# Kernel optimization log

Measured on AMD Instinct MI355X. Metric: run time of the kernel, lower is better.

## Reference

```python
import jax, jax.numpy as jnp
import numpy as np

B, L, ATTN, HID = 1024, 512, 1000, 1000

def setup_inputs() -> dict:
    key = jax.random.key(0)
    k = jax.random.split(key, 5)
    return {
        "hc": jax.random.normal(k[0], (B, HID), dtype=jnp.float32),
        "ho": jax.random.normal(k[1], (B, L, ATTN), dtype=jnp.float32),
        "mask": jnp.zeros((B, L), dtype=bool),
        "Wa_w": jax.random.normal(k[2], (1, ATTN), dtype=jnp.float32) / np.sqrt(ATTN),
        "Wa_b": jnp.zeros((1,), dtype=jnp.float32),
        "Wc_w": jax.random.normal(k[3], (HID, HID + ATTN), dtype=jnp.float32) / np.sqrt(HID + ATTN),
        "Wc_b": jnp.zeros((HID,), dtype=jnp.float32),
    }

def reference(hc, ho, mask, Wa_w, Wa_b, Wc_w, Wc_b):
    # scores: Wa(ho) -> [B, L], then mask + softmax over L
    scores = jnp.einsum('bld,od->bl', ho, Wa_w) + Wa_b[0]
    scores = jnp.where(mask, -10000.0, scores)
    a = jax.nn.softmax(scores, axis=-1)            # [B, L]
    c = jnp.einsum('bl,bld->bd', a, ho)            # context [B, ATTN]
    # dropout in eval mode (identity); concat + output projection
    h = jnp.concatenate([hc, c], axis=1) @ Wc_w.T + Wc_b  # [B, HID]
    return h
```

## Files before the change

### kernel.cpp

```cpp
#include <hip/hip_runtime.h>

#define NB 1024
#define NL 512
#define ND 1000
#define NH 1000

__device__ __forceinline__ void async_copy16(const void* g, void* l) {
    __builtin_amdgcn_global_load_lds(
        (const __attribute__((address_space(1))) void*)g,
        (__attribute__((address_space(3))) void*)l, 16, 0, 0);
}

__global__ __launch_bounds__(256, 4) void attn_pool_kernel(
    const float* __restrict__ ho,
    const unsigned char* __restrict__ mask,
    const float* __restrict__ Wa_w,
    const float* __restrict__ Wa_b,
    float* __restrict__ ctx)
{
    __shared__ __align__(16) char lbuf[4][2][4096];
    __shared__ unsigned char msk[NL];
    __shared__ float mArr[4], sArr[4];

    const int b    = blockIdx.x;
    const int tid  = threadIdx.x;
    const int wave = tid >> 6;
    const int lane = tid & 63;

    const unsigned char* mb = mask + (size_t)b * NL;
    msk[tid]       = mb[tid];
    msk[tid + 256] = mb[tid + 256];

    float4 wa[4];
    #pragma unroll
    for (int j = 0; j < 4; ++j) {
        int slot = lane + 64 * j;
        wa[j] = (slot < 250) ? ((const float4*)Wa_w)[slot] : make_float4(0.f, 0.f, 0.f, 0.f);
    }
    const float bias = Wa_b[0];

    const char* gb   = (const char*)(ho + (size_t)b * (NL * ND));
    const char* gend = (const char*)ho + ((size_t)NB * NL * ND) * 4 - 16;

    __syncthreads();

    auto stageRow = [&](int d, int l) {
        const char* rp = gb + (size_t)l * 4000;
        char* lb = &lbuf[wave][d][0];
        #pragma unroll
        for (int s4 = 0; s4 < 4; ++s4) {
            const char* p = rp + s4 * 1024 + lane * 16;
            if (p > gend) p = gend;
            async_copy16((const void*)p, (void*)(lb + s4 * 1024));
        }
    };

    float  m = -1e30f, s = 0.f;
    float4 acc[4];
    #pragma unroll
    for (int j = 0; j < 4; ++j) acc[j] = make_float4(0.f, 0.f, 0.f, 0.f);

    stageRow(0, wave);

    #pragma unroll 1
    for (int c = 0; c < 128; ++c) {
        if (c + 1 < 128) {
            stageRow((c + 1) & 1, 4 * (c + 1) + wave);
            asm volatile("s_waitcnt vmcnt(4)" ::: "memory");
        } else {
            asm volatile("s_waitcnt vmcnt(0)" ::: "memory");
        }
        __builtin_amdgcn_sched_barrier(0);

        const float4* row = (const float4*)&lbuf[wave][c & 1][0];
        float4 v[4];
        float p = 0.f;
        #pragma unroll
        for (int j = 0; j < 4; ++j) {
            int slot = lane + 64 * j;
            v[j] = (slot < 250) ? row[slot] : make_float4(0.f, 0.f, 0.f, 0.f);
            p += v[j].x * wa[j].x + v[j].y * wa[j].y + v[j].z * wa[j].z + v[j].w * wa[j].w;
        }
        #pragma unroll
        for (int off = 32; off > 0; off >>= 1) p += __shfl_xor(p, off, 64);

        int l = 4 * c + wave;
        float sc = p + bias;
        if (msk[l]) sc = -10000.f;

        float mn = fmaxf(m, sc);
        if (mn > m) {
            float f = __expf(m - mn);
            s *= f;
            #pragma unroll
            for (int j = 0; j < 4; ++j) {
                acc[j].x *= f; acc[j].y *= f; acc[j].z *= f; acc[j].w *= f;
            }
            m = mn;
        }
        float w = __expf(sc - m);
        s += w;
        #pragma unroll
        for (int j = 0; j < 4; ++j) {
            acc[j].x += w * v[j].x; acc[j].y += w * v[j].y;
            acc[j].z += w * v[j].z; acc[j].w += w * v[j].w;
        }
        __builtin_amdgcn_sched_barrier(0);
    }

    __syncthreads();

    float4* cacc4 = (float4*)&lbuf[0][0][0];
    #pragma unroll
    for (int j = 0; j < 4; ++j) {
        int slot = lane + 64 * j;
        if (slot < 250) cacc4[wave * 250 + slot] = acc[j];
    }
    if (lane == 0) { mArr[wave] = m; sArr[wave] = s; }
    __syncthreads();

    float gm = fmaxf(fmaxf(mArr[0], mArr[1]), fmaxf(mArr[2], mArr[3]));
    float f0 = __expf(mArr[0] - gm), f1 = __expf(mArr[1] - gm);
    float f2 = __expf(mArr[2] - gm), f3 = __expf(mArr[3] - gm);
    float S  = f0 * sArr[0] + f1 * sArr[1] + f2 * sArr[2] + f3 * sArr[3];
    float inv = 1.0f / S;

    if (tid < 250) {
        float4 a0 = cacc4[tid], a1 = cacc4[250 + tid], a2 = cacc4[500 + tid], a3 = cacc4[750 + tid];
        float4 r;
        r.x = (f0 * a0.x + f1 * a1.x + f2 * a2.x + f3 * a3.x) * inv;
        r.y = (f0 * a0.y + f1 * a1.y + f2 * a2.y + f3 * a3.y) * inv;
        r.z = (f0 * a0.z + f1 * a1.z + f2 * a2.z + f3 * a3.z) * inv;
        r.w = (f0 * a0.w + f1 * a1.w + f2 * a2.w + f3 * a3.w) * inv;
        ((float4*)(ctx + (size_t)b * ND))[tid] = r;
    }
}

#define KS     4
#define KSLICE 500
#define KT     32

__global__ __launch_bounds__(256, 4) void proj_partial_kernel(
    const float* __restrict__ hc,
    const float* __restrict__ ctx,
    const float* __restrict__ W,
    float* __restrict__ partial)
{
    __shared__ __align__(16) float Xs[16][68];
    __shared__ __align__(16) float Ws[16][68];

    const int tid  = threadIdx.x;
    const int tx   = tid & 15, ty = tid >> 4;
    const int jL   = tid & 15, rL = tid >> 4;
    const int row0 = blockIdx.x * 64;
    const int col0 = blockIdx.y * 64;
    const int k0   = blockIdx.z * KSLICE;

    float acc[4][4] = {{0.f}};

    auto gload = [&](int kt, float* xr, float* wr) {
        int kin = kt * 16 + jL;
        bool ok = kin < KSLICE;
        int kg  = k0 + kin;
        #pragma unroll
        for (int p = 0; p < 4; ++p) {
            int r  = rL + p * 16;
            int gr = row0 + r;
            int go = col0 + r;
            float xv = 0.f, wv = 0.f;
            if (ok) {
                xv = (kg < NH) ? hc[(size_t)gr * NH + kg]
                               : ctx[(size_t)gr * ND + (kg - NH)];
                wv = (go < NH) ? W[(size_t)go * (NH + ND) + kg] : 0.f;
            }
            xr[p] = xv; wr[p] = wv;
        }
    };

    float xr_[4], wr_[4];
    gload(0, xr_, wr_);

    #pragma unroll 1
    for (int kt = 0; kt < KT; ++kt) {
        #pragma unroll
        for (int p = 0; p < 4; ++p) {
            Xs[jL][rL + p * 16] = xr_[p];
            Ws[jL][rL + p * 16] = wr_[p];
        }
        __syncthreads();

        float xn[4], wn[4];
        if (kt + 1 < KT) gload(kt + 1, xn, wn);

        #pragma unroll
        for (int kk = 0; kk < 16; ++kk) {
            float4 xf = *(const float4*)&Xs[kk][ty * 4];
            float4 wf = *(const float4*)&Ws[kk][tx * 4];
            float xq[4] = {xf.x, xf.y, xf.z, xf.w};
            float wq[4] = {wf.x, wf.y, wf.z, wf.w};
            #pragma unroll
            for (int i = 0; i < 4; ++i)
                #pragma unroll
                for (int j = 0; j < 4; ++j)
                    acc[i][j] += xq[i] * wq[j];
        }
        __syncthreads();

        #pragma unroll
        for (int p = 0; p < 4; ++p) { xr_[p] = xn[p]; wr_[p] = wn[p]; }
    }

    float* pbase = partial + (size_t)blockIdx.z * NB * NH;
    #pragma unroll
    for (int i = 0; i < 4; ++i) {
        int gr = row0 + ty * 4 + i;
        int gc = col0 + tx * 4;
        if (gc < NH) {
            float4 o = make_float4(acc[i][0], acc[i][1], acc[i][2], acc[i][3]);
            *(float4*)&pbase[(size_t)gr * NH + gc] = o;
        }
    }
}

__global__ __launch_bounds__(256) void proj_reduce_kernel(
    const float* __restrict__ partial,
    const float* __restrict__ wb,
    float* __restrict__ out)
{
    int idx = blockIdx.x * 256 + threadIdx.x;
    if (idx >= NB * 250) return;
    int bb = idx / 250, j4 = idx - bb * 250;

    float4 r = ((const float4*)wb)[j4];
    #pragma unroll
    for (int s = 0; s < KS; ++s) {
        float4 p = *(const float4*)&partial[((size_t)s * NB + bb) * NH + j4 * 4];
        r.x += p.x; r.y += p.y; r.z += p.z; r.w += p.w;
    }
    *(float4*)&out[(size_t)bb * NH + j4 * 4] = r;
}

extern "C" void kernel_launch(void* const* d_in, const int* in_sizes, int n_in,
                              void* d_out, int out_size, void* d_ws, size_t ws_size,
                              hipStream_t stream) {
    const float* hc           = (const float*)d_in[0];
    const float* ho           = (const float*)d_in[1];
    const unsigned char* mask = (const unsigned char*)d_in[2];
    const float* Wa_w         = (const float*)d_in[3];
    const float* Wa_b         = (const float*)d_in[4];
    const float* Wc_w         = (const float*)d_in[5];
    const float* Wc_b         = (const float*)d_in[6];
    float* out = (float*)d_out;

    float* ctx     = (float*)d_ws;
    float* partial = (float*)d_ws + (size_t)NB * ND;

    attn_pool_kernel<<<NB, 256, 0, stream>>>(ho, mask, Wa_w, Wa_b, ctx);
    proj_partial_kernel<<<dim3(16, 16, KS), 256, 0, stream>>>(hc, ctx, Wc_w, partial);
    proj_reduce_kernel<<<(NB * 250 + 255) / 256, 256, 0, stream>>>(partial, Wc_b, out);
}
```

Before: 431.5 us.

## Replace FP32 split-K projection GEMM with bf16 MFMA kernel and prep conversion

Measured after the change: 388.0 us. -10.1%, faster.

```diff
diff --git a/kernel.cpp b/kernel.cpp
--- a/kernel.cpp
+++ b/kernel.cpp
@@ -4,11 +4,55 @@
 #define NL 512
 #define ND 1000
 #define NH 1000
+#define KP 2048
+
+typedef __attribute__((ext_vector_type(8))) short bf16x8;
+typedef __attribute__((ext_vector_type(4))) float f32x4;
+
+__device__ __forceinline__ unsigned short f2bf(float f) {
+    unsigned u = __float_as_uint(f);
+    u += 0x7FFFu + ((u >> 16) & 1u);
+    return (unsigned short)(u >> 16);
+}
 
 __device__ __forceinline__ void async_copy16(const void* g, void* l) {
     __builtin_amdgcn_global_load_lds(
         (const __attribute__((address_space(1))) void*)g,
         (__attribute__((address_space(3))) void*)l, 16, 0, 0);
+}
+
+__global__ __launch_bounds__(256) void prep_kernel(
+    const float* __restrict__ hc, const float* __restrict__ W,
+    unsigned short* __restrict__ Xb, unsigned short* __restrict__ Wb)
+{
+    const int bid = blockIdx.x, t = threadIdx.x;
+    if (bid < NB) {
+        ushort4* xq = (ushort4*)(Xb + (size_t)bid * KP);
+        if (t < 250) {
+            float4 v = ((const float4*)(hc + (size_t)bid * NH))[t];
+            xq[t] = make_ushort4(f2bf(v.x), f2bf(v.y), f2bf(v.z), f2bf(v.w));
+        } else if (t < 262) {
+            xq[500 + (t - 250)] = make_ushort4(0, 0, 0, 0);
+        }
+    } else {
+        const int n = bid - NB;
+        ushort4* wq = (ushort4*)(Wb + (size_t)n * KP);
+        if (n < NH) {
+            #pragma unroll
+            for (int rep = 0; rep < 2; ++rep) {
+                int q = t + rep * 256;
+                if (q < 500) {
+                    float4 v = ((const float4*)(W + (size_t)n * (NH + ND)))[q];
+                    wq[q] = make_ushort4(f2bf(v.x), f2bf(v.y), f2bf(v.z), f2bf(v.w));
+                } else {
+                    wq[q] = make_ushort4(0, 0, 0, 0);
+                }
+            }
+        } else {
+            wq[t]       = make_ushort4(0, 0, 0, 0);
+            wq[t + 256] = make_ushort4(0, 0, 0, 0);
+        }
+    }
 }
 
 __global__ __launch_bounds__(256, 4) void attn_pool_kernel(
@@ -16,7 +60,7 @@
     const unsigned char* __restrict__ mask,
     const float* __restrict__ Wa_w,
     const float* __restrict__ Wa_b,
-    float* __restrict__ ctx)
+    unsigned short* __restrict__ Xb)
 {
     __shared__ __align__(16) char lbuf[4][2][4096];
     __shared__ unsigned char msk[NL];
@@ -132,112 +176,96 @@
         r.y = (f0 * a0.y + f1 * a1.y + f2 * a2.y + f3 * a3.y) * inv;
         r.z = (f0 * a0.z + f1 * a1.z + f2 * a2.z + f3 * a3.z) * inv;
         r.w = (f0 * a0.w + f1 * a1.w + f2 * a2.w + f3 * a3.w) * inv;
-        ((float4*)(ctx + (size_t)b * ND))[tid] = r;
-    }
-}
-
-#define KS     4
-#define KSLICE 500
-#define KT     32
-
-__global__ __launch_bounds__(256, 4) void proj_partial_kernel(
-    const float* __restrict__ hc,
-    const float* __restrict__ ctx,
-    const float* __restrict__ W,
-    float* __restrict__ partial)
-{
-    __shared__ __align__(16) float Xs[16][68];
-    __shared__ __align__(16) float Ws[16][68];
-
-    const int tid  = threadIdx.x;
-    const int tx   = tid & 15, ty = tid >> 4;
-    const int jL   = tid & 15, rL = tid >> 4;
-    const int row0 = blockIdx.x * 64;
-    const int col0 = blockIdx.y * 64;
-    const int k0   = blockIdx.z * KSLICE;
-
-    float acc[4][4] = {{0.f}};
-
-    auto gload = [&](int kt, float* xr, float* wr) {
-        int kin = kt * 16 + jL;
-        bool ok = kin < KSLICE;
-        int kg  = k0 + kin;
-        #pragma unroll
-        for (int p = 0; p < 4; ++p) {
-            int r  = rL + p * 16;
-            int gr = row0 + r;
-            int go = col0 + r;
-            float xv = 0.f, wv = 0.f;
-            if (ok) {
-                xv = (kg < NH) ? hc[(size_t)gr * NH + kg]
-                               : ctx[(size_t)gr * ND + (kg - NH)];
-                wv = (go < NH) ? W[(size_t)go * (NH + ND) + kg] : 0.f;
-            }
-            xr[p] = xv; wr[p] = wv;
-        }
-    };
-
-    float xr_[4], wr_[4];
-    gload(0, xr_, wr_);
-
-    #pragma unroll 1
-    for (int kt = 0; kt < KT; ++kt) {
-        #pragma unroll
-        for (int p = 0; p < 4; ++p) {
-            Xs[jL][rL + p * 16] = xr_[p];
-            Ws[jL][rL + p * 16] = wr_[p];
-        }
-        __syncthreads();
-
-        float xn[4], wn[4];
-        if (kt + 1 < KT) gload(kt + 1, xn, wn);
-
-        #pragma unroll
-        for (int kk = 0; kk < 16; ++kk) {
-            float4 xf = *(const float4*)&Xs[kk][ty * 4];
-            float4 wf = *(const float4*)&Ws[kk][tx * 4];
-            float xq[4] = {xf.x, xf.y, xf.z, xf.w};
-            float wq[4] = {wf.x, wf.y, wf.z, wf.w};
-            #pragma unroll
-            for (int i = 0; i < 4; ++i)
-                #pragma unroll
-                for (int j = 0; j < 4; ++j)
-                    acc[i][j] += xq[i] * wq[j];
-        }
-        __syncthreads();
-
-        #pragma unroll
-        for (int p = 0; p < 4; ++p) { xr_[p] = xn[p]; wr_[p] = wn[p]; }
-    }
-
-    float* pbase = partial + (size_t)blockIdx.z * NB * NH;
-    #pragma unroll
-    for (int i = 0; i < 4; ++i) {
-        int gr = row0 + ty * 4 + i;
-        int gc = col0 + tx * 4;
-        if (gc < NH) {
-            float4 o = make_float4(acc[i][0], acc[i][1], acc[i][2], acc[i][3]);
-            *(float4*)&pbase[(size_t)gr * NH + gc] = o;
-        }
-    }
-}
-
-__global__ __launch_bounds__(256) void proj_reduce_kernel(
-    const float* __restrict__ partial,
+        ((ushort4*)(Xb + (size_t)b * KP + ND))[tid] =
+            make_ushort4(f2bf(r.x), f2bf(r.y), f2bf(r.z), f2bf(r.w));
+    }
+}
+
+__global__ __launch_bounds__(256, 1) void mfma_proj_kernel(
+    const unsigned short* __restrict__ Xb,
+    const unsigned short* __restrict__ Wb,
     const float* __restrict__ wb,
     float* __restrict__ out)
 {
-    int idx = blockIdx.x * 256 + threadIdx.x;
-    if (idx >= NB * 250) return;
-    int bb = idx / 250, j4 = idx - bb * 250;
-
-    float4 r = ((const float4*)wb)[j4];
-    #pragma unroll
-    for (int s = 0; s < KS; ++s) {
-        float4 p = *(const float4*)&partial[((size_t)s * NB + bb) * NH + j4 * 4];
-        r.x += p.x; r.y += p.y; r.z += p.z; r.w += p.w;
-    }
-    *(float4*)&out[(size_t)bb * NH + j4 * 4] = r;
+    __shared__ float red[64][65];
+
+    const int tid  = threadIdx.x;
+    const int wave = tid >> 6;
+    const int lane = tid & 63;
+    const int row0 = blockIdx.x * 64;
+    const int col0 = blockIdx.y * 64;
+    const int r    = lane & 15;
+    const int g    = lane >> 4;
+
+    const int kbase = wave * 512 + g * 8;
+    const unsigned short* xp = Xb + (size_t)(row0 + r) * KP + kbase;
+    const unsigned short* wp = Wb + (size_t)(col0 + r) * KP + kbase;
+
+    f32x4 acc[4][4];
+    #pragma unroll
+    for (int mi = 0; mi < 4; ++mi)
+        #pragma unroll
+        for (int ni = 0; ni < 4; ++ni)
+            acc[mi][ni] = (f32x4){0.f, 0.f, 0.f, 0.f};
+
+    bf16x8 a_[4], b_[4], an[4], bn[4];
+    #pragma unroll
+    for (int i = 0; i < 4; ++i) {
+        a_[i] = *(const bf16x8*)(xp + (size_t)i * 16 * KP);
+        b_[i] = *(const bf16x8*)(wp + (size_t)i * 16 * KP);
+    }
+
+    #pragma unroll 1
+    for (int ks = 0; ks < 16; ++ks) {
+        if (ks + 1 < 16) {
+            const unsigned short* xq = xp + (ks + 1) * 32;
+            const unsigned short* wq = wp + (ks + 1) * 32;
+            #pragma unroll
+            for (int i = 0; i < 4; ++i) {
+                an[i] = *(const bf16x8*)(xq + (size_t)i * 16 * KP);
+                bn[i] = *(const bf16x8*)(wq + (size_t)i * 16 * KP);
+            }
+        }
+        #pragma unroll
+        for (int mi = 0; mi < 4; ++mi)
+            #pragma unroll
+            for (int ni = 0; ni < 4; ++ni)
+                acc[mi][ni] = __builtin_amdgcn_mfma_f32_16x16x32_bf16(
+                    a_[mi], b_[ni], acc[mi][ni], 0, 0, 0);
+        #pragma unroll
+        for (int i = 0; i < 4; ++i) { a_[i] = an[i]; b_[i] = bn[i]; }
+    }
+
+    #pragma unroll
+    for (int w = 0; w < 4; ++w) {
+        if (wave == w) {
+            #pragma unroll
+            for (int mi = 0; mi < 4; ++mi)
+                #pragma unroll
+                for (int ni = 0; ni < 4; ++ni)
+                    #pragma unroll
+                    for (int j = 0; j < 4; ++j) {
+                        int rr = mi * 16 + g * 4 + j;
+                        int cc = ni * 16 + r;
+                        float v = acc[mi][ni][j];
+                        if (w == 0) red[rr][cc] = v;
+                        else        red[rr][cc] += v;
+                    }
+        }
+        __syncthreads();
+    }
+
+    const int cc = tid & 63;
+    const int rg = tid >> 6;
+    const int gc = col0 + cc;
+    if (gc < NH) {
+        float bias = wb[gc];
+        #pragma unroll
+        for (int i = 0; i < 16; ++i) {
+            int rr = rg * 16 + i;
+            out[(size_t)(row0 + rr) * NH + gc] = red[rr][cc] + bias;
+        }
+    }
 }
 
 extern "C" void kernel_launch(void* const* d_in, const int* in_sizes, int n_in,
@@ -252,10 +280,10 @@
     const float* Wc_b         = (const float*)d_in[6];
     float* out = (float*)d_out;
 
-    float* ctx     = (float*)d_ws;
-    float* partial = (float*)d_ws + (size_t)NB * ND;
-
-    attn_pool_kernel<<<NB, 256, 0, stream>>>(ho, mask, Wa_w, Wa_b, ctx);
-    proj_partial_kernel<<<dim3(16, 16, KS), 256, 0, stream>>>(hc, ctx, Wc_w, partial);
-    proj_reduce_kernel<<<(NB * 250 + 255) / 256, 256, 0, stream>>>(partial, Wc_b, out);
-}
+    unsigned short* Xb = (unsigned short*)d_ws;
+    unsigned short* Wb = (unsigned short*)d_ws + (size_t)NB * KP;
+
+    prep_kernel<<<2048, 256, 0, stream>>>(hc, Wc_w, Xb, Wb);
+    attn_pool_kernel<<<NB, 256, 0, stream>>>(ho, mask, Wa_w, Wa_b, Xb);
+    mfma_proj_kernel<<<dim3(16, 16), 256, 0, stream>>>(Xb, Wb, Wc_b, out);
+}
```
